# Performance work log

Measured on AMD Instinct MI355X. Metric: run time of the kernel, lower is better.

Reference implementation:

```python
import jax, jax.numpy as jnp
import numpy as np

B, N, K = 8, 4096, 20          # clouds, points per cloud, knn neighbors
IN_C, OUT_C = 3, 64            # xyz coords -> feature channels


def setup_inputs() -> dict:
    key = jax.random.key(0)
    k1, k2 = jax.random.split(key, 2)
    x = jax.random.normal(k1, (B * N, IN_C), dtype=jnp.float32)
    batch = (jnp.arange(B * N, dtype=jnp.int32) // N)  # [0..0,1..1,...] equal-size clouds
    # EdgeConv MLP: Linear(2*in_channels -> out_channels) + ReLU
    W = jax.random.normal(k2, (2 * IN_C, OUT_C), dtype=jnp.float32) / jnp.sqrt(jnp.float32(2 * IN_C))
    b = jnp.zeros((OUT_C,), dtype=jnp.float32)
    return {"x": x, "batch": batch, "W": W, "b": b}


def _knn_idx(xr):
    # xr: [B, N, C] -> neighbor indices [B, N, K] (self excluded, like knn_graph loop=False)
    sq = jnp.sum(xr * xr, axis=-1)                                  # [B, N]
    d = sq[:, :, None] + sq[:, None, :] - 2.0 * jnp.einsum("bnd,bmd->bnm", xr, xr)  # [B,N,N]
    ar = jnp.arange(N)
    d = d.at[:, ar, ar].set(jnp.inf)                                 # exclude self-loops
    _, idx = jax.lax.top_k(-d, K)                                    # k smallest distances
    return idx


def reference(x, batch, W, b):
    # batch encodes B equal-size clouds of N points each (constant structure)
    xr = x.reshape(B, N, IN_C)
    idx = _knn_idx(xr)                                               # [B, N, K]
    x_j = jax.vmap(lambda pts, i: pts[i])(xr, idx)                   # gather neighbors [B,N,K,C]
    x_i = xr[:, :, None, :]                                          # center points   [B,N,1,C]
    msg = jnp.concatenate([jnp.broadcast_to(x_i, x_j.shape), x_j - x_i], axis=-1)  # [B,N,K,2C]
    h = jax.nn.relu(jnp.einsum("bnkc,co->bnko", msg, W) + b)         # EdgeConv MLP
    out = jnp.max(h, axis=2)                                         # max aggregation over K
    return out.reshape(B * N, OUT_C)
```

## Files before the change

### kernel.cpp

```cpp
#include <hip/hip_runtime.h>
#include <math.h>

#define NN    4096
#define KK    20
#define QQ    4
#define WAVES 4
#define BLK   (WAVES*64)
#define PPB   (WAVES*QQ)
#define PIT   16
#define CAP   56
#define BPB   (NN/PPB)
#define BB    8

typedef float f32x4 __attribute__((ext_vector_type(4)));
typedef float f32x2 __attribute__((ext_vector_type(2)));

__device__ __forceinline__ unsigned fkey(float f) {
  unsigned u = __float_as_uint(f);
  return u ^ ((unsigned)((int)u >> 31) | 0x80000000u);
}
__device__ __forceinline__ float fkey_inv(unsigned k) {
  unsigned u = (k & 0x80000000u) ? (k ^ 0x80000000u) : ~k;
  return __uint_as_float(u);
}

__global__ void prep_kernel(const float* __restrict__ x,
                            float4* __restrict__ ws4,
                            f32x4* __restrict__ wspk) {
  const int p = blockIdx.x * 256 + threadIdx.x;
  const float* s = x + (size_t)p * 6;
  const float x0 = s[0], y0 = s[1], z0 = s[2];
  const float x1 = s[3], y1 = s[4], z1 = s[5];
  const float w0 = fmaf(z0, z0, fmaf(y0, y0, x0 * x0));
  const float w1 = fmaf(z1, z1, fmaf(y1, y1, x1 * x1));
  ws4[2 * p]     = make_float4(x0, y0, z0, w0);
  ws4[2 * p + 1] = make_float4(x1, y1, z1, w1);
  wspk[2 * p]     = (f32x4){x0, x1, y0, y1};
  wspk[2 * p + 1] = (f32x4){z0, z1, w0, w1};
}

template<bool WS>
__global__ __launch_bounds__(BLK, 8)
void edgeconv_kernel(const float* __restrict__ x,
                     const float4* __restrict__ ws4,
                     const f32x4* __restrict__ wspk,
                     const float* __restrict__ W,
                     const float* __restrict__ bias,
                     float* __restrict__ out) {
  __shared__ float2 cand[PPB][CAP + 1];
  __shared__ int    jkeep[PPB][21];
  __shared__ int    pc[PPB];
  __shared__ int    pk[PPB];

  const int tid  = threadIdx.x;
  const int lane = tid & 63;
  const int w    = tid >> 6;
  const int bb   = blockIdx.x % BB;
  const int blk  = blockIdx.x / BB;
  const int base = bb * NN;
  const int g0   = w * QQ;
  const int myp0 = blk * PPB + g0;

  f32x2 nxp[QQ], nyp[QQ], nzp[QQ];
  #pragma unroll
  for (int q = 0; q < QQ; ++q) {
    const float* p = x + (size_t)(base + myp0 + q) * 3;
    const float a = -2.f * p[0], b = -2.f * p[1], c = -2.f * p[2];
    nxp[q] = (f32x2){a, a}; nyp[q] = (f32x2){b, b}; nzp[q] = (f32x2){c, c};
  }

  if (tid < PPB) { pc[tid] = 0; pk[tid] = 0; }
  __syncthreads();

  auto ldpair = [&](int pr, f32x4& A, f32x4& Bv) {
    if constexpr (WS) {
      A  = wspk[base + (pr << 1)];
      Bv = wspk[base + (pr << 1) + 1];
    } else {
      const float* s = x + ((size_t)base + ((size_t)pr << 1)) * 3;
      const float x0 = s[0], y0 = s[1], z0 = s[2];
      const float x1 = s[3], y1 = s[4], z1 = s[5];
      A  = (f32x4){x0, x1, y0, y1};
      Bv = (f32x4){z0, z1, fmaf(z0, z0, fmaf(y0, y0, x0 * x0)),
                           fmaf(z1, z1, fmaf(y1, y1, x1 * x1))};
    }
  };
  auto ldp = [&](int j) -> float4 {
    if constexpr (WS) {
      return ws4[base + j];
    } else {
      const float* p = x + (size_t)(base + j) * 3;
      const float a = p[0], b = p[1], c = p[2];
      return make_float4(a, b, c, fmaf(c, c, fmaf(b, b, a * a)));
    }
  };
  auto pdist = [&](int q, const f32x4& A, const f32x4& Bv) -> f32x2 {
    return __builtin_elementwise_fma(nxp[q], A.xy,
            __builtin_elementwise_fma(nyp[q], A.zw,
             __builtin_elementwise_fma(nzp[q], Bv.xy, Bv.zw)));
  };

  float m[QQ];
  #pragma unroll
  for (int q = 0; q < QQ; ++q) m[q] = INFINITY;
  #pragma unroll 1
  for (int i = 0; i < PIT; ++i) {
    f32x4 A0, B0, A1, B1;
    ldpair((2 * i + 0) * 64 + lane, A0, B0);
    ldpair((2 * i + 1) * 64 + lane, A1, B1);
    #pragma unroll
    for (int q = 0; q < QQ; ++q) {
      const f32x2 dA = pdist(q, A0, B0);
      const f32x2 dB = pdist(q, A1, B1);
      m[q] = fminf(fminf(m[q], fminf(dA.x, dA.y)), fminf(dB.x, dB.y));
    }
  }

  float tau[QQ];
  #pragma unroll
  for (int q = 0; q < QQ; ++q) {
    const unsigned kp = fkey(m[q]) >> 16;
    unsigned lo = 0u, hi = 0xFFFFu;
    for (int b = 0; b < 16; ++b) {
      const unsigned mid = lo + ((hi - lo) >> 1);
      const unsigned long long bal = __ballot(kp <= mid);
      if (__popcll(bal) > KK) hi = mid; else lo = mid + 1;
    }
    tau[q] = fkey_inv((lo << 16) | 0xFFFFu);
  }

  #pragma unroll 1
  for (int i = 0; i < PIT; ++i) {
    const int pr0 = (2 * i + 0) * 64 + lane;
    const int pr1 = (2 * i + 1) * 64 + lane;
    f32x4 A0, B0, A1, B1;
    ldpair(pr0, A0, B0);
    ldpair(pr1, A1, B1);
    #pragma unroll
    for (int q = 0; q < QQ; ++q) {
      const f32x2 dA = pdist(q, A0, B0);
      const f32x2 dB = pdist(q, A1, B1);
      if (dA.x <= tau[q]) { const int wp = atomicAdd(&pc[g0 + q], 1);
        if (wp < CAP) cand[g0 + q][wp] = make_float2(dA.x, __int_as_float(2 * pr0)); }
      if (dA.y <= tau[q]) { const int wp = atomicAdd(&pc[g0 + q], 1);
        if (wp < CAP) cand[g0 + q][wp] = make_float2(dA.y, __int_as_float(2 * pr0 + 1)); }
      if (dB.x <= tau[q]) { const int wp = atomicAdd(&pc[g0 + q], 1);
        if (wp < CAP) cand[g0 + q][wp] = make_float2(dB.x, __int_as_float(2 * pr1)); }
      if (dB.y <= tau[q]) { const int wp = atomicAdd(&pc[g0 + q], 1);
        if (wp < CAP) cand[g0 + q][wp] = make_float2(dB.y, __int_as_float(2 * pr1 + 1)); }
    }
  }
  __syncthreads();

  {
    const int g   = tid >> 4;
    const int k0  = tid & 15;
    const int myp = blk * PPB + g;
    const int n0  = pc[g];
    const int n   = n0 < CAP ? n0 : CAP;
    for (int k = k0; k < n; k += 16) {
      const float2 ck = cand[g][k];
      const float dk = ck.x; const int jk = __float_as_int(ck.y);
      int rank = 0;
      for (int k2 = 0; k2 < n; ++k2) {
        const float2 c2 = cand[g][k2];
        rank += (c2.x < dk || (c2.x == dk && __float_as_int(c2.y) < jk)) ? 1 : 0;
      }
      if (jk != myp && rank <= KK) jkeep[g][atomicAdd(&pk[g], 1)] = jk;
    }
  }
  __syncthreads();

  const float w3 = W[3*64+lane], w4 = W[4*64+lane], w5 = W[5*64+lane];
  const float c0 = W[0*64+lane] - w3;
  const float c1 = W[1*64+lane] - w4;
  const float c2 = W[2*64+lane] - w5;
  const float bo = bias[lane];

  for (int pi = 0; pi < QQ; ++pi) {
    const int p   = g0 + pi;
    const int pid = blk * PPB + p;
    const float4 xi = ldp(pid);
    const float ci = fmaf(xi.x, c0, fmaf(xi.y, c1, fmaf(xi.z, c2, bo)));
    float hmax = -INFINITY;
    #pragma unroll 5
    for (int k = 0; k < KK; ++k) {
      const int j = __builtin_amdgcn_readfirstlane(jkeep[p][k]);
      const float4 xp = ldp(j);
      hmax = fmaxf(hmax, fmaf(xp.x, w3, fmaf(xp.y, w4, fmaf(xp.z, w5, ci))));
    }
    out[(size_t)(base + pid) * 64 + lane] = fmaxf(hmax, 0.0f);
  }
}

extern "C" void kernel_launch(void* const* d_in, const int* in_sizes, int n_in,
                              void* d_out, int out_size, void* d_ws, size_t ws_size,
                              hipStream_t stream) {
  const float* x  = (const float*)d_in[0];
  const float* W  = (const float*)d_in[2];
  const float* b  = (const float*)d_in[3];
  float* out = (float*)d_out;

  const size_t aosz = (size_t)BB * NN * sizeof(float4);
  const size_t need = 2 * aosz;
  dim3 grid(BB * BPB);
  dim3 block(BLK);
  if (ws_size >= need) {
    float4* ws4 = (float4*)d_ws;
    f32x4* wspk = (f32x4*)((char*)d_ws + aosz);
    hipLaunchKernelGGL(prep_kernel, dim3(BB * NN / 2 / 256), dim3(256), 0, stream,
                       x, ws4, wspk);
    hipLaunchKernelGGL((edgeconv_kernel<true>), grid, block, 0, stream,
                       x, ws4, wspk, W, b, out);
  } else {
    hipLaunchKernelGGL((edgeconv_kernel<false>), grid, block, 0, stream,
                       x, (const float4*)nullptr, (const f32x4*)nullptr, W, b, out);
  }
}
```

Measured before the change: 71.63 us.

## Rescan only lanes whose partial minimum passes the threshold in candidate pass

The second distance pass no longer recomputes all pair distances for every query. Instead it ballots which lane buckets (strided subsets of points) have a per-lane minimum at or below tau, and assigns each qualifying (query, bucket) pair to one lane. That lane rescans only its 32 pairs and appends candidates. This avoids recomputing distances for buckets that cannot contribute, at the cost of gather-style strided loads, bit-select arithmetic and possible divergence across rounds.

```diff
diff --git a/kernel.cpp b/kernel.cpp
--- a/kernel.cpp
+++ b/kernel.cpp
@@ -94,11 +94,6 @@
       return make_float4(a, b, c, fmaf(c, c, fmaf(b, b, a * a)));
     }
   };
-  auto pdist = [&](int q, const f32x4& A, const f32x4& Bv) -> f32x2 {
-    return __builtin_elementwise_fma(nxp[q], A.xy,
-            __builtin_elementwise_fma(nyp[q], A.zw,
-             __builtin_elementwise_fma(nzp[q], Bv.xy, Bv.zw)));
-  };
 
   float m[QQ];
   #pragma unroll
@@ -110,8 +105,12 @@
     ldpair((2 * i + 1) * 64 + lane, A1, B1);
     #pragma unroll
     for (int q = 0; q < QQ; ++q) {
-      const f32x2 dA = pdist(q, A0, B0);
-      const f32x2 dB = pdist(q, A1, B1);
+      const f32x2 dA = __builtin_elementwise_fma(nxp[q], A0.xy,
+                        __builtin_elementwise_fma(nyp[q], A0.zw,
+                         __builtin_elementwise_fma(nzp[q], B0.xy, B0.zw)));
+      const f32x2 dB = __builtin_elementwise_fma(nxp[q], A1.xy,
+                        __builtin_elementwise_fma(nyp[q], A1.zw,
+                         __builtin_elementwise_fma(nzp[q], B1.xy, B1.zw)));
       m[q] = fminf(fminf(m[q], fminf(dA.x, dA.y)), fminf(dB.x, dB.y));
     }
   }
@@ -129,25 +128,67 @@
     tau[q] = fkey_inv((lo << 16) | 0xFFFFu);
   }
 
-  #pragma unroll 1
-  for (int i = 0; i < PIT; ++i) {
-    const int pr0 = (2 * i + 0) * 64 + lane;
-    const int pr1 = (2 * i + 1) * 64 + lane;
-    f32x4 A0, B0, A1, B1;
-    ldpair(pr0, A0, B0);
-    ldpair(pr1, A1, B1);
-    #pragma unroll
-    for (int q = 0; q < QQ; ++q) {
-      const f32x2 dA = pdist(q, A0, B0);
-      const f32x2 dB = pdist(q, A1, B1);
-      if (dA.x <= tau[q]) { const int wp = atomicAdd(&pc[g0 + q], 1);
-        if (wp < CAP) cand[g0 + q][wp] = make_float2(dA.x, __int_as_float(2 * pr0)); }
-      if (dA.y <= tau[q]) { const int wp = atomicAdd(&pc[g0 + q], 1);
-        if (wp < CAP) cand[g0 + q][wp] = make_float2(dA.y, __int_as_float(2 * pr0 + 1)); }
-      if (dB.x <= tau[q]) { const int wp = atomicAdd(&pc[g0 + q], 1);
-        if (wp < CAP) cand[g0 + q][wp] = make_float2(dB.x, __int_as_float(2 * pr1)); }
-      if (dB.y <= tau[q]) { const int wp = atomicAdd(&pc[g0 + q], 1);
-        if (wp < CAP) cand[g0 + q][wp] = make_float2(dB.y, __int_as_float(2 * pr1 + 1)); }
+  {
+    const unsigned long long b0 = __ballot(m[0] <= tau[0]);
+    const unsigned long long b1 = __ballot(m[1] <= tau[1]);
+    const unsigned long long b2 = __ballot(m[2] <= tau[2]);
+    const unsigned long long b3 = __ballot(m[3] <= tau[3]);
+    const int c0 = __popcll(b0);
+    const int c1 = c0 + __popcll(b1);
+    const int c2 = c1 + __popcll(b2);
+    const int c3 = c2 + __popcll(b3);
+    const int rounds = (c3 + 63) >> 6;
+
+    #pragma unroll 1
+    for (int rd = 0; rd < rounds; ++rd) {
+      const int t = (rd << 6) + lane;
+      if (t < c3) {
+        const int q = (t >= c0) + (t >= c1) + (t >= c2);
+        int r = t - (q == 0 ? 0 : (q == 1 ? c0 : (q == 2 ? c1 : c2)));
+        unsigned long long bq = (q == 0) ? b0 : ((q == 1) ? b1 : ((q == 2) ? b2 : b3));
+        int b = 0;
+        {
+          int h = __popcll(bq & 0xFFFFFFFFull);
+          if (r >= h) { b += 32; r -= h; bq >>= 32; }
+          unsigned v = (unsigned)bq;
+          h = __popc(v & 0xFFFFu); if (r >= h) { b += 16; r -= h; v >>= 16; }
+          h = __popc(v & 0xFFu);   if (r >= h) { b += 8;  r -= h; v >>= 8;  }
+          h = __popc(v & 0xFu);    if (r >= h) { b += 4;  r -= h; v >>= 4;  }
+          h = __popc(v & 0x3u);    if (r >= h) { b += 2;  r -= h; v >>= 2;  }
+          h = v & 1u;              if (r >= h) { b += 1; }
+        }
+        const f32x2 cnx = (q & 2) ? ((q & 1) ? nxp[3] : nxp[2])
+                                  : ((q & 1) ? nxp[1] : nxp[0]);
+        const f32x2 cny = (q & 2) ? ((q & 1) ? nyp[3] : nyp[2])
+                                  : ((q & 1) ? nyp[1] : nyp[0]);
+        const f32x2 cnz = (q & 2) ? ((q & 1) ? nzp[3] : nzp[2])
+                                  : ((q & 1) ? nzp[1] : nzp[0]);
+        const float ct  = (q & 2) ? ((q & 1) ? tau[3] : tau[2])
+                                  : ((q & 1) ? tau[1] : tau[0]);
+        const int row = g0 + q;
+        #pragma unroll 1
+        for (int k = 0; k < 32; k += 2) {
+          const int pr0 = (k + 0) * 64 + b;
+          const int pr1 = (k + 1) * 64 + b;
+          f32x4 A0, B0, A1, B1;
+          ldpair(pr0, A0, B0);
+          ldpair(pr1, A1, B1);
+          const f32x2 dA = __builtin_elementwise_fma(cnx, A0.xy,
+                            __builtin_elementwise_fma(cny, A0.zw,
+                             __builtin_elementwise_fma(cnz, B0.xy, B0.zw)));
+          const f32x2 dB = __builtin_elementwise_fma(cnx, A1.xy,
+                            __builtin_elementwise_fma(cny, A1.zw,
+                             __builtin_elementwise_fma(cnz, B1.xy, B1.zw)));
+          if (dA.x <= ct) { const int wp = atomicAdd(&pc[row], 1);
+            if (wp < CAP) cand[row][wp] = make_float2(dA.x, __int_as_float(2 * pr0)); }
+          if (dA.y <= ct) { const int wp = atomicAdd(&pc[row], 1);
+            if (wp < CAP) cand[row][wp] = make_float2(dA.y, __int_as_float(2 * pr0 + 1)); }
+          if (dB.x <= ct) { const int wp = atomicAdd(&pc[row], 1);
+            if (wp < CAP) cand[row][wp] = make_float2(dB.x, __int_as_float(2 * pr1)); }
+          if (dB.y <= ct) { const int wp = atomicAdd(&pc[row], 1);
+            if (wp < CAP) cand[row][wp] = make_float2(dB.y, __int_as_float(2 * pr1 + 1)); }
+        }
+      }
     }
   }
   __syncthreads();
```

Result: slower. 93.24 us (+30.2%).
